# Performance work log

Hardware: AMD Instinct MI355X
Metric: run time of the kernel (lower is better)

## Reference

```python
import jax, jax.numpy as jnp
import numpy as np

P = 10          # num_vars (agents)
DIM = 2         # out_dims (2D)
K = 5           # order
H = 256         # hidden_layer_size
INPUT_DIM = 40  # per-agent feature block
ND = DIM + (P - 1) * DIM  # num_dims_model = 20
OUT = ND * DIM            # per-net MLP output = 40
T = 20000


def _gather_idx():
    # per-agent selected features: [pos(dim), relpos (p-1)*dim] (skips vel at offset dim..2*dim)
    base = np.arange(P) * INPUT_DIM
    a = np.arange(DIM)[None, :] + base[:, None]                      # (P, dim)
    b = np.arange(2 * DIM, (2 + P - 1) * DIM)[None, :] + base[:, None]  # (P, (p-1)*dim)
    return np.concatenate([a, b], axis=1)  # (P, ND)


def _fp_idx():
    i = np.arange(P)[:, None]
    j = np.arange(P - 1)[None, :]
    indd = (i + 1) * INPUT_DIM - (P - 1) + j        # last (p-1) entries of block i
    indd2 = indd - (P - 1)                          # preceding (p-1) entries
    return indd, indd2


def setup_inputs() -> dict:
    key = jax.random.key(0)
    ks = jax.random.split(key, 8)
    s = 0.05
    return {
        "inputs": jax.random.normal(ks[0], (T, K, P * INPUT_DIM), dtype=jnp.float32),
        "W1": jax.random.normal(ks[1], (K, P, ND, H), dtype=jnp.float32) * s,
        "b1": jnp.zeros((K, P, H), dtype=jnp.float32),
        "W2": jax.random.normal(ks[2], (K, P, H, H), dtype=jnp.float32) * s,
        "b2": jnp.zeros((K, P, H), dtype=jnp.float32),
        "W3": jax.random.normal(ks[3], (K, P, H, OUT), dtype=jnp.float32) * s,
        "b3": jnp.zeros((K, P, OUT), dtype=jnp.float32),
        "avoid": jnp.asarray(0.1, dtype=jnp.float32),  # avoid_nets.bias (bat init)
    }


def reference(inputs, W1, b1, W2, b2, W3, b3, avoid):
    Tl = inputs.shape[0]
    idx = _gather_idx()
    indd, indd2 = _fp_idx()

    # pairwise perceptual gating, 'bat' branch (uses avoid bias)
    xlast = inputs[:, -1, :]                       # (T, P*INPUT_DIM)
    xF = xlast[:, indd]                            # (T, P, P-1)
    xF2 = xlast[:, indd2]                          # (T, P, P-1)
    coeffs_FP = jax.nn.sigmoid(100.0 * (xF - avoid)) * (jax.nn.sigmoid(100.0 * xF2) - 0.5) * 2.0

    # grouped per-(k,i) MLPs, batched via einsum
    sel = inputs[:, :, idx]                        # (T, K, P, ND)
    h = jax.nn.relu(jnp.einsum('tkpn,kpnh->tkph', sel, W1) + b1)
    h = jax.nn.relu(jnp.einsum('tkph,kphg->tkpg', h, W2) + b2)
    c = jnp.einsum('tkpg,kpgo->tkpo', h, W3) + b3  # (T, K, P, OUT)
    c = (c ** 2).reshape(Tl, K, P, DIM, ND)        # percept: squared coeffs

    # gate last (p-1)*dim coefficient columns by coeffs_FP (repeated dim times)
    gate = jnp.repeat(coeffs_FP, DIM, axis=-1)     # (T, P, (P-1)*DIM)
    mult = jnp.concatenate([jnp.ones((Tl, P, DIM), dtype=c.dtype), gate], axis=-1)  # (T, P, ND)
    c2 = c * mult[:, None, :, None, :]             # (T, K, P, DIM, ND)

    preds = jnp.einsum('tkpon,tkpn->tpo', c2, sel).reshape(Tl, P * DIM)
    coeffs = c2.reshape(Tl, K, P * DIM, ND)
    return preds, coeffs, coeffs_FP
```

## Files before the change

kernel.cpp:

```cpp
#include <hip/hip_runtime.h>
#include <hip/hip_bf16.h>

#define Kn   5
#define Pn   10
#define Hn   256
#define NDn  20
#define OUTn 40
#define INDn 40
#define ROWn 400
#define TT   32
#define CSTRIDE 52

typedef float  f32x4  __attribute__((ext_vector_type(4)));
typedef float  f32x2  __attribute__((ext_vector_type(2)));
typedef short  bf16x8 __attribute__((ext_vector_type(8)));
typedef unsigned int u32;
typedef unsigned short u16;

#define W1B_OFF 0
#define W1B_PER 8192
#define W2B_OFF 409600
#define W2B_PER 65536
#define W3B_OFF 3686400
#define W3B_PER 12288
#define WS_ELEMS 4300800
#define WS_BYTES (WS_ELEMS * 2)

__device__ __forceinline__ u16 f2bf(float f) {
    u32 u = __float_as_uint(f);
    return (u16)((u + 0x7fffu + ((u >> 16) & 1u)) >> 16);
}

__device__ __forceinline__ u32 cvt_pk_bf16(float a, float b) {
    u32 r;
    asm("v_cvt_pk_bf16_f32 %0, %1, %2" : "=v"(r) : "v"(a), "v"(b));
    return r;
}

__global__ void prep_weights(const float* __restrict__ W1, const float* __restrict__ W2,
                             const float* __restrict__ W3, const float* __restrict__ inputs,
                             const float* __restrict__ avoid_p,
                             float* __restrict__ cfp, short* __restrict__ ws, int T) {
    int sid = blockIdx.x * 256 + threadIdx.x;
    const float* src; int e, kst, n, ss, kmax, ng, nmax; size_t obase;
    if (sid < 51200) {
        e = sid >> 10; int r = sid & 1023; n = r >> 2; ss = r & 3; kst = 0;
        src = W1 + (size_t)e * (NDn * Hn); kmax = NDn; ng = Hn; nmax = Hn;
        obase = W1B_OFF + (size_t)e * W1B_PER;
    } else if (sid < 460800) {
        int s = sid - 51200; e = s >> 13; int r = s & 8191;
        kst = r >> 10; int rr = r & 1023; n = rr >> 2; ss = rr & 3;
        src = W2 + (size_t)e * (Hn * Hn); kmax = Hn; ng = Hn; nmax = Hn;
        obase = W2B_OFF + (size_t)e * W2B_PER + (size_t)kst * 8192;
    } else if (sid < 537600) {
        int s = sid - 460800; e = s / 1536; int r = s - e * 1536;
        kst = r / 192; int rr = r - kst * 192; n = rr >> 2; ss = rr & 3;
        src = W3 + (size_t)e * (Hn * OUTn); kmax = Hn; ng = OUTn; nmax = OUTn;
        obase = W3B_OFF + (size_t)e * W3B_PER + (size_t)kst * 1536;
    } else {
        int g = sid - 537600;
        if (g < T * (Pn * (Pn - 1))) {
            int t = g / 90, rm = g - t * 90;
            int pp = rm / 9, j = rm - pp * 9;
            size_t base = ((size_t)t * Kn + (Kn - 1)) * ROWn + pp * INDn;
            float xF  = inputs[base + 31 + j];
            float xF2 = inputs[base + 22 + j];
            float s1 = 1.0f / (1.0f + __expf(-100.0f * (xF - *avoid_p)));
            float s2 = 1.0f / (1.0f + __expf(-100.0f * xF2));
            cfp[g] = s1 * (s2 - 0.5f) * 2.0f;
        }
        return;
    }

    u16 v[8];
    #pragma unroll
    for (int j = 0; j < 8; ++j) {
        int k = kst * 32 + ss * 8 + j;
        float f = (k < kmax && n < nmax) ? src[(size_t)k * ng + n] : 0.0f;
        v[j] = f2bf(f);
    }
    u32 q0 = (u32)v[0] | ((u32)v[1] << 16), q1 = (u32)v[2] | ((u32)v[3] << 16);
    u32 q2 = (u32)v[4] | ((u32)v[5] << 16), q3 = (u32)v[6] | ((u32)v[7] << 16);
    *(uint4*)(ws + obase + (size_t)n * 32 + ss * 8) = make_uint4(q0, q1, q2, q3);
}

__device__ __forceinline__ void epi_store_h(short* hA_, const f32x4 (*A)[4],
                                            int wid, int lane) {
    const int lg = lane >> 4, lr = lane & 15;
    #pragma unroll
    for (int mt = 0; mt < 2; ++mt) {
        #pragma unroll
        for (int r = 0; r < 4; ++r) {
            const int t = 16 * mt + 4 * lg + r;
            #pragma unroll
            for (int nt = 0; nt < 4; ++nt) {
                float vv = fmaxf(A[mt][nt][r], 0.0f);
                u32 pk = cvt_pk_bf16(vv, vv);
                int col = 64 * wid + 16 * nt + lr;
                int off = t * 512 + ((2 * col) ^ ((t & 7) << 4));
                *reinterpret_cast<u16*>(reinterpret_cast<char*>(hA_) + off) = (u16)pk;
            }
        }
    }
}

template<int KS>
__device__ __forceinline__ void c_step(const char* w2, const short* hA_, int wid,
                                       int lg, int lr, bf16x8 (&cur)[4], bf16x8 (&nxt)[4],
                                       f32x4 (&acc)[2][4]) {
    if (KS < 7) {
        #pragma unroll
        for (int nt = 0; nt < 4; ++nt) {
            int n = 64 * wid + 16 * nt + lr;
            nxt[nt] = *(const bf16x8*)(w2 + (KS + 1) * 16384 + n * 64 + lg * 16);
        }
    }
    bf16x8 aF[2];
    #pragma unroll
    for (int mt = 0; mt < 2; ++mt) {
        int t = 16 * mt + lr;
        aF[mt] = *(const bf16x8*)((const char*)hA_ + t * 512 + ((KS * 64 + lg * 16) ^ ((t & 7) << 4)));
    }
    __builtin_amdgcn_s_setprio(1);
    #pragma unroll
    for (int mt = 0; mt < 2; ++mt)
        #pragma unroll
        for (int nt = 0; nt < 4; ++nt)
            acc[mt][nt] = __builtin_amdgcn_mfma_f32_16x16x32_bf16(aF[mt], cur[nt], acc[mt][nt], 0, 0, 0);
    __builtin_amdgcn_s_setprio(0);
}

template<int KS>
__device__ __forceinline__ void d_step(const char* w3, const short* hA_, int t, int ncnt,
                                       int nbase, int lg, int lr,
                                       bf16x8 (&cur)[2], bf16x8 (&nxt)[2], f32x4 (&accd)[2]) {
    if (KS < 7) {
        #pragma unroll
        for (int j = 0; j < 2; ++j)
            if (j < ncnt) {
                int n = 16 * (nbase + j) + lr;
                nxt[j] = *(const bf16x8*)(w3 + (KS + 1) * 3072 + n * 64 + lg * 16);
            }
    }
    bf16x8 aF = *(const bf16x8*)((const char*)hA_ + t * 512 + ((KS * 64 + lg * 16) ^ ((t & 7) << 4)));
    __builtin_amdgcn_s_setprio(1);
    #pragma unroll
    for (int j = 0; j < 2; ++j)
        if (j < ncnt)
            accd[j] = __builtin_amdgcn_mfma_f32_16x16x32_bf16(aF, cur[j], accd[j], 0, 0, 0);
    __builtin_amdgcn_s_setprio(0);
}

__launch_bounds__(256, 4)
__global__ void senngc_mfma(const float* __restrict__ inputs,
                            const float* __restrict__ b1, const float* __restrict__ b2,
                            const float* __restrict__ b3,
                            const float* __restrict__ cfp_in,
                            const short* __restrict__ ws,
                            float* __restrict__ preds, float* __restrict__ coeffs, int T)
{
    __shared__ __align__(16) short selA[TT * 32];
    __shared__ __align__(16) short hA[TT * Hn];
    __shared__ u16  sh_mult[TT][NDn];

    const int tid  = threadIdx.x;

    const int NB   = gridDim.x;
    const int nch  = NB / (Pn * Kn);
    const int bx   = blockIdx.x & 7, bj = blockIdx.x >> 3;
    const int bbase = NB >> 3, brem = NB & 7;
    const int L    = bx * bbase + (bx < brem ? bx : brem) + bj;
    const int pair = L / nch;
    const int t0   = (L - pair * nch) * TT;
    const int p    = pair / Kn;
    const int ke   = pair - p * Kn;

    const int wid  = tid >> 6, lane = tid & 63;
    const int lg   = lane >> 4, lr = lane & 15;

    const int e = ke * Pn + p;
    const char* w1 = (const char*)(ws + W1B_OFF + (size_t)e * W1B_PER);
    const char* w2 = (const char*)(ws + W2B_OFF + (size_t)e * W2B_PER);
    const char* w3 = (const char*)(ws + W3B_OFF + (size_t)e * W3B_PER);

    if (tid < 128) {
        int row = tid >> 2, ss = tid & 3;
        int kg = ss ^ ((row >> 1) & 3);
        int trow = (t0 + row < T) ? (t0 + row) : (T - 1);
        const float* src = inputs + ((size_t)trow * Kn + ke) * ROWn + p * INDn;
        int c0 = kg ? (kg * 8 + 2) : 0;
        int o1 = kg ? (c0 + 2) : 4;
        int o2 = kg ? (c0 + 4) : 6;
        int o3 = kg ? (c0 + 6) : 8;
        f32x2 va = *(const f32x2*)(src + c0);
        f32x2 vb = *(const f32x2*)(src + o1);
        f32x2 vc = *(const f32x2*)(src + o2);
        f32x2 vd = *(const f32x2*)(src + o3);
        float f[8] = {va[0], va[1], vb[0], vb[1], vc[0], vc[1], vd[0], vd[1]};
        #pragma unroll
        for (int j = 0; j < 8; ++j)
            if (kg * 8 + j >= NDn) f[j] = 0.0f;
        u32 q0 = cvt_pk_bf16(f[0], f[1]), q1 = cvt_pk_bf16(f[2], f[3]);
        u32 q2 = cvt_pk_bf16(f[4], f[5]), q3 = cvt_pk_bf16(f[6], f[7]);
        *(uint4*)((char*)selA + row * 64 + ss * 16) = make_uint4(q0, q1, q2, q3);
    }

    if (tid < 32) *(u32*)&sh_mult[tid][0] = 0x3F803F80u;
    {
        int r = tid / 9, j = tid - r * 9;
        if (tid < TT * (Pn - 1)) {
            float cf = (t0 + r < T) ? cfp_in[(size_t)(t0 + r) * (Pn * (Pn - 1)) + p * (Pn - 1) + j] : 0.0f;
            *(u32*)&sh_mult[r][2 + 2 * j] = cvt_pk_bf16(cf, cf);
        }
        int i2 = tid + 256;
        if (i2 < TT * (Pn - 1)) {
            int r2 = i2 / 9, j2 = i2 - r2 * 9;
            float cf = (t0 + r2 < T) ? cfp_in[(size_t)(t0 + r2) * (Pn * (Pn - 1)) + p * (Pn - 1) + j2] : 0.0f;
            *(u32*)&sh_mult[r2][2 + 2 * j2] = cvt_pk_bf16(cf, cf);
        }
    }

    bf16x8 bW[4];
    float bias1[4], bias2[4];
    #pragma unroll
    for (int nt = 0; nt < 4; ++nt) {
        int n = 64 * wid + 16 * nt + lr;
        bW[nt] = *(const bf16x8*)(w1 + n * 64 + lg * 16);
        bias1[nt] = b1[e * Hn + n];
        bias2[nt] = b2[e * Hn + n];
    }
    __syncthreads();

    f32x4 acc[2][4];

    #pragma unroll
    for (int mt = 0; mt < 2; ++mt)
        #pragma unroll
        for (int nt = 0; nt < 4; ++nt)
            acc[mt][nt] = (f32x4){bias1[nt], bias1[nt], bias1[nt], bias1[nt]};
    {
        bf16x8 aS[2];
        #pragma unroll
        for (int mt = 0; mt < 2; ++mt) {
            int t = 16 * mt + lr;
            aS[mt] = *(const bf16x8*)((const char*)selA + t * 64 + ((lg ^ ((t >> 1) & 3)) << 4));
        }
        __builtin_amdgcn_s_setprio(1);
        #pragma unroll
        for (int mt = 0; mt < 2; ++mt)
            #pragma unroll
            for (int nt = 0; nt < 4; ++nt)
                acc[mt][nt] = __builtin_amdgcn_mfma_f32_16x16x32_bf16(aS[mt], bW[nt], acc[mt][nt], 0, 0, 0);
        __builtin_amdgcn_s_setprio(0);
    }
    bf16x8 bA[4], bB[4];
    #pragma unroll
    for (int nt = 0; nt < 4; ++nt) {
        int n = 64 * wid + 16 * nt + lr;
        bA[nt] = *(const bf16x8*)(w2 + n * 64 + lg * 16);
    }
    epi_store_h(hA, acc, wid, lane);
    __syncthreads();

    #pragma unroll
    for (int mt = 0; mt < 2; ++mt)
        #pragma unroll
        for (int nt = 0; nt < 4; ++nt)
            acc[mt][nt] = (f32x4){bias2[nt], bias2[nt], bias2[nt], bias2[nt]};
    c_step<0>(w2, hA, wid, lg, lr, bA, bB, acc);
    c_step<1>(w2, hA, wid, lg, lr, bB, bA, acc);
    c_step<2>(w2, hA, wid, lg, lr, bA, bB, acc);
    c_step<3>(w2, hA, wid, lg, lr, bB, bA, acc);
    c_step<4>(w2, hA, wid, lg, lr, bA, bB, acc);
    c_step<5>(w2, hA, wid, lg, lr, bB, bA, acc);
    c_step<6>(w2, hA, wid, lg, lr, bA, bB, acc);
    c_step<7>(w2, hA, wid, lg, lr, bB, bA, acc);
    __syncthreads();

    const int mslot = wid >> 1;
    const int nbase = (wid & 1) ? 2 : 0;
    const int ncnt  = (wid & 1) ? 1 : 2;
    const int tD    = 16 * mslot + lr;
    bf16x8 dA[2], dB[2];
    #pragma unroll
    for (int j = 0; j < 2; ++j)
        if (j < ncnt) {
            int n = 16 * (nbase + j) + lr;
            dA[j] = *(const bf16x8*)(w3 + n * 64 + lg * 16);
        }
    epi_store_h(hA, acc, wid, lane);
    __syncthreads();

    {
        f32x4 accd[2];
        accd[0] = (f32x4){0.f, 0.f, 0.f, 0.f};
        accd[1] = (f32x4){0.f, 0.f, 0.f, 0.f};
        d_step<0>(w3, hA, tD, ncnt, nbase, lg, lr, dA, dB, accd);
        d_step<1>(w3, hA, tD, ncnt, nbase, lg, lr, dB, dA, accd);
        d_step<2>(w3, hA, tD, ncnt, nbase, lg, lr, dA, dB, accd);
        d_step<3>(w3, hA, tD, ncnt, nbase, lg, lr, dB, dA, accd);
        d_step<4>(w3, hA, tD, ncnt, nbase, lg, lr, dA, dB, accd);
        d_step<5>(w3, hA, tD, ncnt, nbase, lg, lr, dB, dA, accd);
        d_step<6>(w3, hA, tD, ncnt, nbase, lg, lr, dA, dB, accd);
        d_step<7>(w3, hA, tD, ncnt, nbase, lg, lr, dB, dA, accd);
        __syncthreads();
        {
            float* cst = (float*)hA;
            #pragma unroll
            for (int j = 0; j < 2; ++j)
                if (j < ncnt)
                    #pragma unroll
                    for (int r = 0; r < 4; ++r)
                        cst[(16 * mslot + 4 * lg + r) * CSTRIDE + 16 * (nbase + j) + lr] = accd[j][r];
        }
    }
    __syncthreads();

    {
        const float* cst = (const float*)hA;
        const int r  = tid >> 3, g = tid & 7;
        const int d  = g >> 2;
        const int o0 = 5 * g;
        const int n0 = 5 * (g & 3);
        float s = 0.0f;
        if (t0 + r < T) {
            const float* bb3 = b3 + e * OUTn + o0;
            float* crow = coeffs + (((size_t)(t0 + r) * Kn + ke) * Pn + p) * OUTn + o0;
            #pragma unroll
            for (int j = 0; j < 5; ++j) {
                float c = cst[r * CSTRIDE + o0 + j] + bb3[j];
                int n = n0 + j;
                float m = __uint_as_float((u32)sh_mult[r][n] << 16);
                float c2 = c * c * m;
                crow[j] = c2;
                int offs = r * 64 + (((n >> 3) ^ ((r >> 1) & 3)) << 4) + (n & 7) * 2;
                u16 u = *(const u16*)((const char*)selA + offs);
                s = fmaf(c2, __uint_as_float((u32)u << 16), s);
            }
        }
        s += __shfl_xor(s, 1);
        s += __shfl_xor(s, 2);
        if ((g & 3) == 0 && t0 + r < T)
            atomicAdd(&preds[(size_t)(t0 + r) * (Pn * 2) + p * 2 + d], s);
    }
}

#define FMA4(ACC, A, W)              \
    ACC.x = fmaf(A.x, W, ACC.x);     \
    ACC.y = fmaf(A.y, W, ACC.y);     \
    ACC.z = fmaf(A.z, W, ACC.z);     \
    ACC.w = fmaf(A.w, W, ACC.w);

__launch_bounds__(256, 4)
__global__ void senngc_fused_f32(const float* __restrict__ inputs,
                                 const float* __restrict__ W1, const float* __restrict__ b1,
                                 const float* __restrict__ W2, const float* __restrict__ b2,
                                 const float* __restrict__ W3, const float* __restrict__ b3,
                                 const float* __restrict__ avoid_p,
                                 float* __restrict__ preds, float* __restrict__ coeffs,
                                 float* __restrict__ cfp, int T)
{
    __shared__ __align__(16) float lds_T[Hn * 32];
    __shared__ __align__(16) float selT[NDn * 32];
    __shared__ float sh_mult[32][NDn];
    __shared__ float sh_pred[32][2];

    const int tid = threadIdx.x;
    const int p   = blockIdx.y;
    const int t0  = blockIdx.x * 32;
    const float avoid = *avoid_p;

    if (tid < 64) {
        sh_pred[tid >> 1][tid & 1] = 0.0f;
        sh_mult[tid >> 1][tid & 1] = 1.0f;
    }
    for (int i = tid; i < 32 * (Pn - 1); i += 256) {
        int r = i / 9, j = i - r * 9;
        float cf = 0.0f;
        if (t0 + r < T) {
            size_t base = ((size_t)(t0 + r) * Kn + (Kn - 1)) * ROWn + p * INDn;
            float xF  = inputs[base + 31 + j];
            float xF2 = inputs[base + 22 + j];
            float s1 = 1.0f / (1.0f + __expf(-100.0f * (xF - avoid)));
            float s2 = 1.0f / (1.0f + __expf(-100.0f * xF2));
            cf = s1 * (s2 - 0.5f) * 2.0f;
            cfp[(size_t)(t0 + r) * (Pn * (Pn - 1)) + p * (Pn - 1) + j] = cf;
        }
        sh_mult[r][2 + 2 * j] = cf;
        sh_mult[r][3 + 2 * j] = cf;
    }

    const int tr = tid >> 5;
    const int tc = tid & 31;
    float4 acc[8];

    for (int k = 0; k < Kn; ++k) {
        __syncthreads();
        for (int i = tid; i < NDn * 32; i += 256) {
            int n = i >> 5, r = i & 31;
            float v = 0.0f;
            if (t0 + r < T) {
                int col = p * INDn + (n < 2 ? n : n + 2);
                v = inputs[((size_t)(t0 + r) * Kn + k) * ROWn + col];
            }
            selT[n * 32 + r] = v;
        }
        __syncthreads();
        {
            const float* w1 = W1 + (size_t)(k * Pn + p) * NDn * Hn;
            const float* bb = b1 + (k * Pn + p) * Hn;
            float4 bv0 = *(const float4*)(bb + 8 * tc);
            float4 bv1 = *(const float4*)(bb + 8 * tc + 4);
            acc[0] = make_float4(bv0.x, bv0.x, bv0.x, bv0.x);
            acc[1] = make_float4(bv0.y, bv0.y, bv0.y, bv0.y);
            acc[2] = make_float4(bv0.z, bv0.z, bv0.z, bv0.z);
            acc[3] = make_float4(bv0.w, bv0.w, bv0.w, bv0.w);
            acc[4] = make_float4(bv1.x, bv1.x, bv1.x, bv1.x);
            acc[5] = make_float4(bv1.y, bv1.y, bv1.y, bv1.y);
            acc[6] = make_float4(bv1.z, bv1.z, bv1.z, bv1.z);
            acc[7] = make_float4(bv1.w, bv1.w, bv1.w, bv1.w);
            #pragma unroll 4
            for (int kk = 0; kk < NDn; ++kk) {
                float4 a = *(const float4*)&selT[kk * 32 + 4 * tr];
                const float* wr = w1 + kk * Hn + 8 * tc;
                float4 w0  = *(const float4*)(wr);
                float4 w1v = *(const float4*)(wr + 4);
                FMA4(acc[0], a, w0.x);  FMA4(acc[1], a, w0.y);
                FMA4(acc[2], a, w0.z);  FMA4(acc[3], a, w0.w);
                FMA4(acc[4], a, w1v.x); FMA4(acc[5], a, w1v.y);
                FMA4(acc[6], a, w1v.z); FMA4(acc[7], a, w1v.w);
            }
            #pragma unroll
            for (int c = 0; c < 8; ++c) {
                int col = 8 * tc + c;
                float4 v = acc[c];
                v.x = fmaxf(v.x, 0.0f); v.y = fmaxf(v.y, 0.0f);
                v.z = fmaxf(v.z, 0.0f); v.w = fmaxf(v.w, 0.0f);
                *(float4*)&lds_T[col * 32 + ((4 * tr) ^ ((col & 7) << 2))] = v;
            }
        }
        __syncthreads();
        {
            const float* w2 = W2 + (size_t)(k * Pn + p) * Hn * Hn;
            const float* bb = b2 + (k * Pn + p) * Hn;
            float4 bv0 = *(const float4*)(bb + 8 * tc);
            float4 bv1 = *(const float4*)(bb + 8 * tc + 4);
            acc[0] = make_float4(bv0.x, bv0.x, bv0.x, bv0.x);
            acc[1] = make_float4(bv0.y, bv0.y, bv0.y, bv0.y);
            acc[2] = make_float4(bv0.z, bv0.z, bv0.z, bv0.z);
            acc[3] = make_float4(bv0.w, bv0.w, bv0.w, bv0.w);
            acc[4] = make_float4(bv1.x, bv1.x, bv1.x, bv1.x);
            acc[5] = make_float4(bv1.y, bv1.y, bv1.y, bv1.y);
            acc[6] = make_float4(bv1.z, bv1.z, bv1.z, bv1.z);
            acc[7] = make_float4(bv1.w, bv1.w, bv1.w, bv1.w);
            #pragma unroll 2
            for (int kk = 0; kk < Hn; ++kk) {
                float4 a = *(const float4*)&lds_T[kk * 32 + ((4 * tr) ^ ((kk & 7) << 2))];
                const float* wr = w2 + kk * Hn + 8 * tc;
                float4 w0  = *(const float4*)(wr);
                float4 w1v = *(const float4*)(wr + 4);
                FMA4(acc[0], a, w0.x);  FMA4(acc[1], a, w0.y);
                FMA4(acc[2], a, w0.z);  FMA4(acc[3], a, w0.w);
                FMA4(acc[4], a, w1v.x); FMA4(acc[5], a, w1v.y);
                FMA4(acc[6], a, w1v.z); FMA4(acc[7], a, w1v.w);
            }
            __syncthreads();
            #pragma unroll
            for (int c = 0; c < 8; ++c) {
                int col = 8 * tc + c;
                float4 v = acc[c];
                v.x = fmaxf(v.x, 0.0f); v.y = fmaxf(v.y, 0.0f);
                v.z = fmaxf(v.z, 0.0f); v.w = fmaxf(v.w, 0.0f);
                *(float4*)&lds_T[col * 32 + ((4 * tr) ^ ((col & 7) << 2))] = v;
            }
        }
        __syncthreads();
        {
            const int kq  = tid >> 6;
            const int tr2 = (tid >> 3) & 7;
            const int cg  = tid & 7;
            const float* w3 = W3 + (size_t)(k * Pn + p) * Hn * OUTn;
            float accd[4][5];
            #pragma unroll
            for (int a_ = 0; a_ < 4; ++a_)
                #pragma unroll
                for (int j = 0; j < 5; ++j) accd[a_][j] = 0.0f;
            #pragma unroll 2
            for (int kk = kq * 64; kk < kq * 64 + 64; ++kk) {
                float4 a = *(const float4*)&lds_T[kk * 32 + ((4 * tr2) ^ ((kk & 7) << 2))];
                const float* wr = w3 + kk * OUTn + 5 * cg;
                #pragma unroll
                for (int j = 0; j < 5; ++j) {
                    float w = wr[j];
                    accd[0][j] = fmaf(a.x, w, accd[0][j]);
                    accd[1][j] = fmaf(a.y, w, accd[1][j]);
                    accd[2][j] = fmaf(a.z, w, accd[2][j]);
                    accd[3][j] = fmaf(a.w, w, accd[3][j]);
                }
            }
            __syncthreads();
            #pragma unroll
            for (int r4 = 0; r4 < 4; ++r4)
                #pragma unroll
                for (int j = 0; j < 5; ++j)
                    lds_T[(kq * 32 + 4 * tr2 + r4) * OUTn + 5 * cg + j] = accd[r4][j];
        }
        __syncthreads();
        {
            const float* bb3 = b3 + (k * Pn + p) * OUTn;
            for (int i = tid; i < 32 * OUTn; i += 256) {
                int r = i / OUTn, o = i - r * OUTn;
                if (t0 + r >= T) continue;
                float c = bb3[o]
                        + lds_T[(0 * 32 + r) * OUTn + o]
                        + lds_T[(1 * 32 + r) * OUTn + o]
                        + lds_T[(2 * 32 + r) * OUTn + o]
                        + lds_T[(3 * 32 + r) * OUTn + o];
                int d = (o >= NDn) ? 1 : 0;
                int n = o - d * NDn;
                float c2 = c * c * sh_mult[r][n];
                coeffs[(((size_t)(t0 + r) * Kn + k) * Pn + p) * OUTn + o] = c2;
                atomicAdd(&sh_pred[r][d], c2 * selT[n * 32 + r]);
            }
        }
    }

    __syncthreads();
    if (tid < 64) {
        int r = tid >> 1, d = tid & 1;
        if (t0 + r < T)
            preds[(size_t)(t0 + r) * (Pn * 2) + p * 2 + d] = sh_pred[r][d];
    }
}

extern "C" void kernel_launch(void* const* d_in, const int* in_sizes, int n_in,
                              void* d_out, int out_size, void* d_ws, size_t ws_size,
                              hipStream_t stream) {
    const float* inputs = (const float*)d_in[0];
    const float* W1 = (const float*)d_in[1];
    const float* b1 = (const float*)d_in[2];
    const float* W2 = (const float*)d_in[3];
    const float* b2 = (const float*)d_in[4];
    const float* W3 = (const float*)d_in[5];
    const float* b3 = (const float*)d_in[6];
    const float* avoid = (const float*)d_in[7];
    const int T = in_sizes[0] / (Kn * ROWn);

    float* out    = (float*)d_out;
    float* preds  = out;
    float* coeffs = out + (size_t)T * (Pn * 2);
    float* cfp    = coeffs + (size_t)T * Kn * Pn * OUTn;

    if (ws_size >= (size_t)WS_BYTES) {
        short* ws = (short*)d_ws;
        hipMemsetAsync(preds, 0, (size_t)T * (Pn * 2) * sizeof(float), stream);
        const int prep_items = 537600 + T * (Pn * (Pn - 1));
        hipLaunchKernelGGL(prep_weights, dim3((prep_items + 255) / 256), dim3(256), 0, stream,
                           W1, W2, W3, inputs, avoid, cfp, ws, T);
        const int nch = (T + TT - 1) / TT;
        hipLaunchKernelGGL(senngc_mfma, dim3(nch * Pn * Kn), dim3(256), 0, stream,
                           inputs, b1, b2, b3, cfp, ws, preds, coeffs, T);
    } else {
        dim3 grid((T + 31) / 32, Pn);
        hipLaunchKernelGGL(senngc_fused_f32, grid, dim3(256), 0, stream,
                           inputs, W1, b1, W2, b2, W3, b3, avoid, preds, coeffs, cfp, T);
    }
}
```

Before: 433.2 us.

## Switch second-layer GEMM to 32x32x16 MFMA with 16-row LDS swizzle

The 256x256 hidden layer GEMM now uses 32x32x16 bf16 MFMA tiles, two per wave per K-step over 16 steps, instead of eight 16x16x32 tiles over 8 steps. This halves the A-fragment LDS reads per step and uses the larger MFMA shape, which has better operand reuse. The LDS XOR swizzle on the hidden buffer widens from 8 to 16 rows to suit the new 32-lane access pattern. A new epilogue writes the 32x32 accumulator layout back. The trade-off is longer per-instruction latency and a shorter prefetch distance per step.

```diff
diff --git a/kernel.cpp b/kernel.cpp
--- a/kernel.cpp
+++ b/kernel.cpp
@@ -11,9 +11,10 @@
 #define TT   32
 #define CSTRIDE 52
 
-typedef float  f32x4  __attribute__((ext_vector_type(4)));
-typedef float  f32x2  __attribute__((ext_vector_type(2)));
-typedef short  bf16x8 __attribute__((ext_vector_type(8)));
+typedef float  f32x4   __attribute__((ext_vector_type(4)));
+typedef float  f32x16  __attribute__((ext_vector_type(16)));
+typedef float  f32x2   __attribute__((ext_vector_type(2)));
+typedef short  bf16x8  __attribute__((ext_vector_type(8)));
 typedef unsigned int u32;
 typedef unsigned short u16;
 
@@ -84,8 +85,9 @@
     *(uint4*)(ws + obase + (size_t)n * 32 + ss * 8) = make_uint4(q0, q1, q2, q3);
 }
 
-__device__ __forceinline__ void epi_store_h(short* hA_, const f32x4 (*A)[4],
-                                            int wid, int lane) {
+
+__device__ __forceinline__ void epi_store_h16(short* hA_, const f32x4 (*A)[4],
+                                              int wid, int lane) {
     const int lg = lane >> 4, lr = lane & 15;
     #pragma unroll
     for (int mt = 0; mt < 2; ++mt) {
@@ -97,36 +99,51 @@
                 float vv = fmaxf(A[mt][nt][r], 0.0f);
                 u32 pk = cvt_pk_bf16(vv, vv);
                 int col = 64 * wid + 16 * nt + lr;
-                int off = t * 512 + ((2 * col) ^ ((t & 7) << 4));
+                int off = t * 512 + ((2 * col) ^ ((t & 15) << 4));
                 *reinterpret_cast<u16*>(reinterpret_cast<char*>(hA_) + off) = (u16)pk;
             }
         }
     }
 }
 
+__device__ __forceinline__ void epi_store_h32(short* hA_, const f32x16 (&A)[2],
+                                              int wid, int lane) {
+    const int l31 = lane & 31, g = lane >> 5;
+    #pragma unroll
+    for (int c2 = 0; c2 < 2; ++c2) {
+        #pragma unroll
+        for (int q = 0; q < 16; ++q) {
+            const int row = (q & 3) + 8 * (q >> 2) + 4 * g;
+            float vv = fmaxf(A[c2][q], 0.0f);
+            u32 pk = cvt_pk_bf16(vv, vv);
+            int col = 64 * wid + 32 * c2 + l31;
+            int off = row * 512 + ((2 * col) ^ ((row & 15) << 4));
+            *reinterpret_cast<u16*>(reinterpret_cast<char*>(hA_) + off) = (u16)pk;
+        }
+    }
+}
+
+template<int KS16>
+__device__ __forceinline__ void ld_b32(const char* w2, int wid, int g, int l31,
+                                       bf16x8 (&dst)[2]) {
+    #pragma unroll
+    for (int c2 = 0; c2 < 2; ++c2) {
+        int n = 64 * wid + 32 * c2 + l31;
+        dst[c2] = *(const bf16x8*)(w2 + (KS16 >> 1) * 16384 + n * 64
+                                   + (2 * (KS16 & 1) + g) * 16);
+    }
+}
+
 template<int KS>
-__device__ __forceinline__ void c_step(const char* w2, const short* hA_, int wid,
-                                       int lg, int lr, bf16x8 (&cur)[4], bf16x8 (&nxt)[4],
-                                       f32x4 (&acc)[2][4]) {
-    if (KS < 7) {
-        #pragma unroll
-        for (int nt = 0; nt < 4; ++nt) {
-            int n = 64 * wid + 16 * nt + lr;
-            nxt[nt] = *(const bf16x8*)(w2 + (KS + 1) * 16384 + n * 64 + lg * 16);
-        }
-    }
-    bf16x8 aF[2];
-    #pragma unroll
-    for (int mt = 0; mt < 2; ++mt) {
-        int t = 16 * mt + lr;
-        aF[mt] = *(const bf16x8*)((const char*)hA_ + t * 512 + ((KS * 64 + lg * 16) ^ ((t & 7) << 4)));
-    }
+__device__ __forceinline__ void c32_step(const char* w2, const short* hA_, int wid,
+                                         int g, int l31, bf16x8 (&cur)[2], bf16x8 (&nxt)[2],
+                                         f32x16 (&acc)[2]) {
+    if (KS < 15) ld_b32<(KS < 15 ? KS + 1 : 15)>(w2, wid, g, l31, nxt);
+    bf16x8 aF = *(const bf16x8*)((const char*)hA_ + l31 * 512
+                                 + ((KS * 32 + g * 16) ^ ((l31 & 15) << 4)));
     __builtin_amdgcn_s_setprio(1);
-    #pragma unroll
-    for (int mt = 0; mt < 2; ++mt)
-        #pragma unroll
-        for (int nt = 0; nt < 4; ++nt)
-            acc[mt][nt] = __builtin_amdgcn_mfma_f32_16x16x32_bf16(aF[mt], cur[nt], acc[mt][nt], 0, 0, 0);
+    acc[0] = __builtin_amdgcn_mfma_f32_32x32x16_bf16(aF, cur[0], acc[0], 0, 0, 0);
+    acc[1] = __builtin_amdgcn_mfma_f32_32x32x16_bf16(aF, cur[1], acc[1], 0, 0, 0);
     __builtin_amdgcn_s_setprio(0);
 }
 
@@ -142,7 +159,7 @@
                 nxt[j] = *(const bf16x8*)(w3 + (KS + 1) * 3072 + n * 64 + lg * 16);
             }
     }
-    bf16x8 aF = *(const bf16x8*)((const char*)hA_ + t * 512 + ((KS * 64 + lg * 16) ^ ((t & 7) << 4)));
+    bf16x8 aF = *(const bf16x8*)((const char*)hA_ + t * 512 + ((KS * 64 + lg * 16) ^ ((t & 15) << 4)));
     __builtin_amdgcn_s_setprio(1);
     #pragma unroll
     for (int j = 0; j < 2; ++j)
@@ -177,6 +194,7 @@
 
     const int wid  = tid >> 6, lane = tid & 63;
     const int lg   = lane >> 4, lr = lane & 15;
+    const int l31  = lane & 31, gg = lane >> 5;
 
     const int e = ke * Pn + p;
     const char* w1 = (const char*)(ws + W1B_OFF + (size_t)e * W1B_PER);
@@ -221,14 +239,16 @@
     }
 
     bf16x8 bW[4];
-    float bias1[4], bias2[4];
+    float bias1[4], bias2c[2];
     #pragma unroll
     for (int nt = 0; nt < 4; ++nt) {
         int n = 64 * wid + 16 * nt + lr;
         bW[nt] = *(const bf16x8*)(w1 + n * 64 + lg * 16);
         bias1[nt] = b1[e * Hn + n];
-        bias2[nt] = b2[e * Hn + n];
-    }
+    }
+    #pragma unroll
+    for (int c2 = 0; c2 < 2; ++c2)
+        bias2c[c2] = b2[e * Hn + 64 * wid + 32 * c2 + l31];
     __syncthreads();
 
     f32x4 acc[2][4];
@@ -253,28 +273,33 @@
                 acc[mt][nt] = __builtin_amdgcn_mfma_f32_16x16x32_bf16(aS[mt], bW[nt], acc[mt][nt], 0, 0, 0);
         __builtin_amdgcn_s_setprio(0);
     }
-    bf16x8 bA[4], bB[4];
-    #pragma unroll
-    for (int nt = 0; nt < 4; ++nt) {
-        int n = 64 * wid + 16 * nt + lr;
-        bA[nt] = *(const bf16x8*)(w2 + n * 64 + lg * 16);
-    }
-    epi_store_h(hA, acc, wid, lane);
+    bf16x8 cA[2], cB[2];
+    ld_b32<0>(w2, wid, gg, l31, cA);
+    epi_store_h16(hA, acc, wid, lane);
     __syncthreads();
 
-    #pragma unroll
-    for (int mt = 0; mt < 2; ++mt)
-        #pragma unroll
-        for (int nt = 0; nt < 4; ++nt)
-            acc[mt][nt] = (f32x4){bias2[nt], bias2[nt], bias2[nt], bias2[nt]};
-    c_step<0>(w2, hA, wid, lg, lr, bA, bB, acc);
-    c_step<1>(w2, hA, wid, lg, lr, bB, bA, acc);
-    c_step<2>(w2, hA, wid, lg, lr, bA, bB, acc);
-    c_step<3>(w2, hA, wid, lg, lr, bB, bA, acc);
-    c_step<4>(w2, hA, wid, lg, lr, bA, bB, acc);
-    c_step<5>(w2, hA, wid, lg, lr, bB, bA, acc);
-    c_step<6>(w2, hA, wid, lg, lr, bA, bB, acc);
-    c_step<7>(w2, hA, wid, lg, lr, bB, bA, acc);
+    f32x16 acc32[2];
+    #pragma unroll
+    for (int c2 = 0; c2 < 2; ++c2)
+        #pragma unroll
+        for (int q = 0; q < 16; ++q)
+            acc32[c2][q] = bias2c[c2];
+    c32_step< 0>(w2, hA, wid, gg, l31, cA, cB, acc32);
+    c32_step< 1>(w2, hA, wid, gg, l31, cB, cA, acc32);
+    c32_step< 2>(w2, hA, wid, gg, l31, cA, cB, acc32);
+    c32_step< 3>(w2, hA, wid, gg, l31, cB, cA, acc32);
+    c32_step< 4>(w2, hA, wid, gg, l31, cA, cB, acc32);
+    c32_step< 5>(w2, hA, wid, gg, l31, cB, cA, acc32);
+    c32_step< 6>(w2, hA, wid, gg, l31, cA, cB, acc32);
+    c32_step< 7>(w2, hA, wid, gg, l31, cB, cA, acc32);
+    c32_step< 8>(w2, hA, wid, gg, l31, cA, cB, acc32);
+    c32_step< 9>(w2, hA, wid, gg, l31, cB, cA, acc32);
+    c32_step<10>(w2, hA, wid, gg, l31, cA, cB, acc32);
+    c32_step<11>(w2, hA, wid, gg, l31, cB, cA, acc32);
+    c32_step<12>(w2, hA, wid, gg, l31, cA, cB, acc32);
+    c32_step<13>(w2, hA, wid, gg, l31, cB, cA, acc32);
+    c32_step<14>(w2, hA, wid, gg, l31, cA, cB, acc32);
+    c32_step<15>(w2, hA, wid, gg, l31, cB, cA, acc32);
     __syncthreads();
 
     const int mslot = wid >> 1;
@@ -288,7 +313,7 @@
             int n = 16 * (nbase + j) + lr;
             dA[j] = *(const bf16x8*)(w3 + n * 64 + lg * 16);
         }
-    epi_store_h(hA, acc, wid, lane);
+    epi_store_h32(hA, acc32, wid, lane);
     __syncthreads();
 
     {
```

After: 447.0 us. 3.2% more time.
